# Kernel optimization log

Hardware: AMD Instinct MI355X
Metric: run time of the kernel (lower is better)

## Reference

```python
import jax, jax.numpy as jnp
from jax import lax
import numpy as np

ROUTINGS = 3
NUM_CAPSULE = 8
NUM_ATOMS = 32

def _squash(x):
    # squash(x) = x/||x|| * ||x||^2/(1+||x||^2), norm over last axis
    norm = jnp.linalg.norm(x, axis=-1, keepdims=True)
    norm_sq = norm * norm
    return x / norm * (norm_sq / (1.0 + norm_sq))

def setup_inputs() -> dict:
    key = jax.random.key(0)
    k1, k2, k3 = jax.random.split(key, 3)
    input_tensor = jax.random.normal(k1, (2, 24, 24, 24, 8, 32), dtype=jnp.float32)
    # he_normal-ish scale for conv kernel [k,k,k,in_atoms, C*A]
    fan_in = 3 * 3 * 3 * 32
    W = jax.random.normal(k2, (3, 3, 3, 32, NUM_CAPSULE * NUM_ATOMS), dtype=jnp.float32) * np.sqrt(2.0 / fan_in).astype(np.float32)
    b = jnp.full((1, 1, 1, NUM_CAPSULE, NUM_ATOMS), 0.1, dtype=jnp.float32)
    return {"input_tensor": input_tensor, "W": W, "b": b}

def reference(input_tensor, W, b):
    B, H, Wd, T, IC, IA = input_tensor.shape
    C, A = NUM_CAPSULE, NUM_ATOMS
    # fold input capsule dim into batch: [IC, B, H, W, T, IA] -> [IC*B, H, W, T, IA]
    x = jnp.transpose(input_tensor, (4, 0, 1, 2, 3, 5)).reshape(IC * B, H, Wd, T, IA)
    conv = lax.conv_general_dilated(
        x, W, window_strides=(1, 1, 1), padding='SAME',
        dimension_numbers=('NDHWC', 'DHWIO', 'NDHWC'))  # [IC*B, H, W, T, C*A]
    # reshape exactly as the TF layer does (leading dims relabelled [B, IC])
    votes = conv.reshape(B, IC, H, Wd, T, C, A)
    biases = jnp.broadcast_to(b, (H, Wd, T, C, A))
    logits = jnp.zeros((B, IC, H, Wd, T, C), dtype=votes.dtype)
    activation = None
    for i in range(ROUTINGS):
        route = jax.nn.softmax(logits, axis=-1)                     # [B,IC,H,W,T,C]
        # sum over input capsules of route-weighted votes, plus bias
        preactivate = jnp.sum(route[..., None] * votes, axis=1) + biases  # [B,H,W,T,C,A]
        activation = _squash(preactivate)
        if i < ROUTINGS - 1:
            # agreement update (last-iteration update never affects output)
            distances = jnp.sum(votes * activation[:, None], axis=-1)  # [B,IC,H,W,T,C]
            logits = logits + distances
    return activation
```

## Files before the change

kernel.cpp:

```cpp
#include <hip/hip_runtime.h>
#include <math.h>


#define SPT 13824

typedef __attribute__((ext_vector_type(8))) _Float16 half8;
typedef __attribute__((ext_vector_type(4))) float f32x4;

__device__ __forceinline__ float redhalf(float v) {
  v += __shfl_xor(v, 16);
  v += __shfl_xor(v, 8);
  v += __shfl_xor(v, 4);
  v += __shfl_xor(v, 2);
  v += __shfl_xor(v, 1);
  return v;
}

__global__ void prep_W(const float* __restrict__ W, _Float16* __restrict__ Wh) {
  const int tap = blockIdx.x;
  #pragma unroll
  for (int rep = 0; rep < 4; ++rep) {
    const int idx = rep * 256 + threadIdx.x;
    const int cb = idx >> 6;
    const int kg = (idx >> 4) & 3;
    const int nr = idx & 15;
    const int n  = cb * 16 + nr;
    half8 o;
    #pragma unroll
    for (int j = 0; j < 8; ++j)
      o[j] = (_Float16)W[(tap * 32 + kg * 8 + j) * 256 + n];
    *(half8*)(Wh + tap * 8192 + idx * 8) = o;
  }
}

__global__ __launch_bounds__(256, 4)
void caps_conv(const float* __restrict__ xg, const _Float16* __restrict__ Wh,
               _Float16* __restrict__ vws) {
  __shared__ __align__(16) unsigned char lds[34560];

  const int t    = threadIdx.x;
  const int lane = t & 63;
  const int w    = t >> 6;
  const int wg   = (blockIdx.x & 7) * 432 + (blockIdx.x >> 3);
  const int rbase = wg * 8;
  const int b2   = rbase / SPT;
  const int posb = rbase % SPT;
  const int z  = posb / 576;
  const int y  = (posb % 576) / 24;
  const int x0 = posb % 24;

  const bool stager = t < 240;
  const int sdy  = t / 80;
  const int srem = t % 80;
  const int sxs  = srem >> 3;
  const int sic  = srem & 7;
  const int sn   = b2 * 8 + sic;
  const int sbin = sn & 1;
  const int sicin = sn >> 1;
  const int syy  = y + sdy - 1;
  const int sxx  = x0 + sxs - 1;
  const int sR   = (sdy * 10 + sxs) * 8 + sic;
  const bool syx_ok = (unsigned)syy < 24u && (unsigned)sxx < 24u;
  const float* sbase = xg + (((sbin * 24) * 24 + (syx_ok ? syy : 0)) * 24 + (syx_ok ? sxx : 0)) * 256 + sicin * 32;

  const int lm = lane & 15;
  int abase[4];
  #pragma unroll
  for (int mi = 0; mi < 4; ++mi)
    abase[mi] = ((mi * 2 + (lm >> 3)) * 8 + (lane & 7)) * 72 + (lane >> 4) * 16;

  const _Float16* bbase = Wh + w * 2048 + lane * 8;

  f32x4 acc[4][4];
  #pragma unroll
  for (int mi = 0; mi < 4; ++mi)
    #pragma unroll
    for (int ni = 0; ni < 4; ++ni) acc[mi][ni] = (f32x4){0.f, 0.f, 0.f, 0.f};

  {
    const int zz = z - 1;
    const bool val = (unsigned)zz < 24u && syx_ok;
    const float* src = sbase + (zz >= 0 ? zz : 0) * 24 * 24 * 256;
    half8 h[4];
    #pragma unroll
    for (int j = 0; j < 4; ++j) {
      float4 qa = val ? *(const float4*)(src + j * 8)     : (float4){0,0,0,0};
      float4 qb = val ? *(const float4*)(src + j * 8 + 4) : (float4){0,0,0,0};
      half8 hh;
      hh[0]=(_Float16)qa.x; hh[1]=(_Float16)qa.y; hh[2]=(_Float16)qa.z; hh[3]=(_Float16)qa.w;
      hh[4]=(_Float16)qb.x; hh[5]=(_Float16)qb.y; hh[6]=(_Float16)qb.z; hh[7]=(_Float16)qb.w;
      h[j] = hh;
    }
    if (stager) {
      unsigned char* dst = lds + sR * 72;
      #pragma unroll
      for (int j = 0; j < 4; ++j) *(half8*)(dst + j * 16) = h[j];
    }
  }
  __syncthreads();

  #pragma unroll 1
  for (int dz = 0; dz < 3; ++dz) {
    half8 h[4];
    const bool have = dz < 2;
    {
      const int zz = z + dz;
      const bool val = have && (unsigned)zz < 24u && syx_ok;
      const float* src = sbase + zz * 24 * 24 * 256;
      #pragma unroll
      for (int j = 0; j < 4; ++j) {
        float4 qa = val ? *(const float4*)(src + j * 8)     : (float4){0,0,0,0};
        float4 qb = val ? *(const float4*)(src + j * 8 + 4) : (float4){0,0,0,0};
        half8 hh;
        hh[0]=(_Float16)qa.x; hh[1]=(_Float16)qa.y; hh[2]=(_Float16)qa.z; hh[3]=(_Float16)qa.w;
        hh[4]=(_Float16)qb.x; hh[5]=(_Float16)qb.y; hh[6]=(_Float16)qb.z; hh[7]=(_Float16)qb.w;
        h[j] = hh;
      }
    }

    const unsigned char* sb = lds + (dz & 1) * 17280;
    #pragma unroll 1
    for (int dy = 0; dy < 3; ++dy) {
      const _Float16* bt = bbase + (dz * 9 + dy * 3) * 8192;
      half8 bA0, bA1, bA2, bA3, bB0, bB1, bB2, bB3;
      bA0 = *(const half8*)(bt + 0 * 512);
      bA1 = *(const half8*)(bt + 1 * 512);
      bA2 = *(const half8*)(bt + 2 * 512);
      bA3 = *(const half8*)(bt + 3 * 512);

      bB0 = *(const half8*)(bt + 8192 + 0 * 512);
      bB1 = *(const half8*)(bt + 8192 + 1 * 512);
      bB2 = *(const half8*)(bt + 8192 + 2 * 512);
      bB3 = *(const half8*)(bt + 8192 + 3 * 512);
      {
        const int imm = dy * 5760;
        half8 af[4];
        #pragma unroll
        for (int mi = 0; mi < 4; ++mi) af[mi] = *(const half8*)(sb + abase[mi] + imm);
        #pragma unroll
        for (int mi = 0; mi < 4; ++mi) {
          acc[mi][0] = __builtin_amdgcn_mfma_f32_16x16x32_f16(af[mi], bA0, acc[mi][0], 0, 0, 0);
          acc[mi][1] = __builtin_amdgcn_mfma_f32_16x16x32_f16(af[mi], bA1, acc[mi][1], 0, 0, 0);
          acc[mi][2] = __builtin_amdgcn_mfma_f32_16x16x32_f16(af[mi], bA2, acc[mi][2], 0, 0, 0);
          acc[mi][3] = __builtin_amdgcn_mfma_f32_16x16x32_f16(af[mi], bA3, acc[mi][3], 0, 0, 0);
        }
      }
      bA0 = *(const half8*)(bt + 16384 + 0 * 512);
      bA1 = *(const half8*)(bt + 16384 + 1 * 512);
      bA2 = *(const half8*)(bt + 16384 + 2 * 512);
      bA3 = *(const half8*)(bt + 16384 + 3 * 512);
      {
        const int imm = dy * 5760 + 576;
        half8 af[4];
        #pragma unroll
        for (int mi = 0; mi < 4; ++mi) af[mi] = *(const half8*)(sb + abase[mi] + imm);
        #pragma unroll
        for (int mi = 0; mi < 4; ++mi) {
          acc[mi][0] = __builtin_amdgcn_mfma_f32_16x16x32_f16(af[mi], bB0, acc[mi][0], 0, 0, 0);
          acc[mi][1] = __builtin_amdgcn_mfma_f32_16x16x32_f16(af[mi], bB1, acc[mi][1], 0, 0, 0);
          acc[mi][2] = __builtin_amdgcn_mfma_f32_16x16x32_f16(af[mi], bB2, acc[mi][2], 0, 0, 0);
          acc[mi][3] = __builtin_amdgcn_mfma_f32_16x16x32_f16(af[mi], bB3, acc[mi][3], 0, 0, 0);
        }
      }
      {
        const int imm = dy * 5760 + 1152;
        half8 af[4];
        #pragma unroll
        for (int mi = 0; mi < 4; ++mi) af[mi] = *(const half8*)(sb + abase[mi] + imm);
        #pragma unroll
        for (int mi = 0; mi < 4; ++mi) {
          acc[mi][0] = __builtin_amdgcn_mfma_f32_16x16x32_f16(af[mi], bA0, acc[mi][0], 0, 0, 0);
          acc[mi][1] = __builtin_amdgcn_mfma_f32_16x16x32_f16(af[mi], bA1, acc[mi][1], 0, 0, 0);
          acc[mi][2] = __builtin_amdgcn_mfma_f32_16x16x32_f16(af[mi], bA2, acc[mi][2], 0, 0, 0);
          acc[mi][3] = __builtin_amdgcn_mfma_f32_16x16x32_f16(af[mi], bA3, acc[mi][3], 0, 0, 0);
        }
      }
    }

    if (have && stager) {
      unsigned char* dst = lds + ((dz + 1) & 1) * 17280 + sR * 72;
      #pragma unroll
      for (int j = 0; j < 4; ++j) *(half8*)(dst + j * 16) = h[j];
    }
    __syncthreads();
  }

  _Float16* vb = vws + (size_t)wg * 64 * 256;
  const int rowb = (lane >> 4) * 4;
  const int colb = w * 64 + (lane & 15);
  #pragma unroll
  for (int mi = 0; mi < 4; ++mi)
    #pragma unroll
    for (int ni = 0; ni < 4; ++ni)
      #pragma unroll
      for (int j = 0; j < 4; ++j)
        vb[(size_t)(mi * 16 + rowb + j) * 256 + colb + ni * 16] = (_Float16)acc[mi][ni][j];
}

__global__
void caps_route(const _Float16* __restrict__ vws, const float* __restrict__ bg,
                float* __restrict__ outg) {
  __shared__ float smL[4 * 128];

  const int t    = threadIdx.x;
  const int lane = t & 63;
  const int w    = t >> 6;
  const int grow = blockIdx.x * 4 + w;

  const int ch = lane >> 5;
  const int al = lane & 31;
  float* smLw = smL + w * 128;

  float bia[4];
  #pragma unroll
  for (int q = 0; q < 4; ++q) bia[q] = bg[(2 * q + ch) * 32 + al];

  const _Float16* vp = vws + (size_t)grow * 8 * 256;
  float v[8][4];
  #pragma unroll
  for (int ic = 0; ic < 8; ++ic)
    #pragma unroll
    for (int q = 0; q < 4; ++q)
      v[ic][q] = (float)vp[ic * 256 + (2 * q + ch) * 32 + al];

  #pragma unroll 1
  for (int it = 0; it < 3; ++it) {
    const float* Lrd = smLw + ((it + 1) & 1) * 64;
    float pre[4];
    #pragma unroll
    for (int q = 0; q < 4; ++q) pre[q] = bia[q];
    if (it == 0) {
      #pragma unroll
      for (int ic = 0; ic < 8; ++ic)
        #pragma unroll
        for (int q = 0; q < 4; ++q)
          pre[q] = fmaf(0.125f, v[ic][q], pre[q]);
    } else {
      #pragma unroll
      for (int ic = 0; ic < 8; ++ic) {
        const float4 La = *(const float4*)(Lrd + ic * 8);
        const float4 Lb = *(const float4*)(Lrd + ic * 8 + 4);
        const float Lv[8] = {La.x, La.y, La.z, La.w, Lb.x, Lb.y, Lb.z, Lb.w};
        float mx = Lv[0];
        #pragma unroll
        for (int cc = 1; cc < 8; ++cc) mx = fmaxf(mx, Lv[cc]);
        float e[8];
        float s = 0.f;
        #pragma unroll
        for (int cc = 0; cc < 8; ++cc) { e[cc] = __expf(Lv[cc] - mx); s += e[cc]; }
        const float inv = 1.0f / s;
        #pragma unroll
        for (int q = 0; q < 4; ++q)
          pre[q] = fmaf(e[2 * q + ch] * inv, v[ic][q], pre[q]);
      }
    }

    float act[4];
    #pragma unroll
    for (int q = 0; q < 4; ++q) {
      float ns = redhalf(pre[q] * pre[q]);
      act[q] = pre[q] * (sqrtf(ns) / (1.0f + ns));
    }

    if (it == 2) {
      #pragma unroll
      for (int q = 0; q < 4; ++q)
        outg[(size_t)grow * 256 + (2 * q + ch) * 32 + al] = act[q];
    } else {
      float* Lwr = smLw + (it & 1) * 64;
      #pragma unroll
      for (int ic = 0; ic < 8; ++ic)
        #pragma unroll
        for (int q = 0; q < 4; ++q) {
          float dd = redhalf(v[ic][q] * act[q]);
          if (al == 0) {
            const int cc = 2 * q + ch;
            Lwr[ic * 8 + cc] = (it == 0) ? dd : Lrd[ic * 8 + cc] + dd;
          }
        }
      __syncthreads();
    }
  }
}

__global__ __launch_bounds__(256, 4)
void caps_mfma7(const float* __restrict__ xg, const _Float16* __restrict__ Wh,
                const float* __restrict__ bg, float* __restrict__ outg) {
  __shared__ __align__(16) unsigned char lds[35840];
  float* smV = (float*)lds;

  const int t    = threadIdx.x;
  const int lane = t & 63;
  const int w    = t >> 6;
  const int wg   = (blockIdx.x & 7) * 432 + (blockIdx.x >> 3);
  const int rbase = wg * 8;
  const int b2   = rbase / SPT;
  const int posb = rbase % SPT;
  const int z  = posb / 576;
  const int y  = (posb % 576) / 24;
  const int x0 = posb % 24;

  const bool stager = t < 240;
  const int sdy  = t / 80;
  const int srem = t % 80;
  const int sxs  = srem >> 3;
  const int sic  = srem & 7;
  const int sn   = b2 * 8 + sic;
  const int sbin = sn & 1;
  const int sicin = sn >> 1;
  const int syy  = y + sdy - 1;
  const int sxx  = x0 + sxs - 1;
  const int sR   = (sdy * 10 + sxs) * 8 + sic;
  const bool syx_ok = (unsigned)syy < 24u && (unsigned)sxx < 24u;
  const float* sbase = xg + (((sbin * 24) * 24 + (syx_ok ? syy : 0)) * 24 + (syx_ok ? sxx : 0)) * 256 + sicin * 32;

  const int lm = lane & 15;
  int abase[4];
  #pragma unroll
  for (int mi = 0; mi < 4; ++mi)
    abase[mi] = ((mi * 2 + (lm >> 3)) * 8 + (lane & 7)) * 72 + (lane >> 4) * 16;

  const _Float16* bbase = Wh + w * 2048 + lane * 8;

  f32x4 acc[4][4];
  #pragma unroll
  for (int mi = 0; mi < 4; ++mi)
    #pragma unroll
    for (int ni = 0; ni < 4; ++ni) acc[mi][ni] = (f32x4){0.f, 0.f, 0.f, 0.f};

  {
    const int zz = z - 1;
    const bool val = (unsigned)zz < 24u && syx_ok;
    const float* src = sbase + (zz >= 0 ? zz : 0) * 24 * 24 * 256;
    half8 h[4];
    #pragma unroll
    for (int j = 0; j < 4; ++j) {
      float4 qa = val ? *(const float4*)(src + j * 8)     : (float4){0,0,0,0};
      float4 qb = val ? *(const float4*)(src + j * 8 + 4) : (float4){0,0,0,0};
      half8 hh;
      hh[0]=(_Float16)qa.x; hh[1]=(_Float16)qa.y; hh[2]=(_Float16)qa.z; hh[3]=(_Float16)qa.w;
      hh[4]=(_Float16)qb.x; hh[5]=(_Float16)qb.y; hh[6]=(_Float16)qb.z; hh[7]=(_Float16)qb.w;
      h[j] = hh;
    }
    if (stager) {
      unsigned char* dst = lds + sR * 72;
      #pragma unroll
      for (int j = 0; j < 4; ++j) *(half8*)(dst + j * 16) = h[j];
    }
  }
  __syncthreads();

  #pragma unroll 1
  for (int dz = 0; dz < 3; ++dz) {
    half8 h[4];
    const bool have = dz < 2;
    {
      const int zz = z + dz;
      const bool val = have && (unsigned)zz < 24u && syx_ok;
      const float* src = sbase + zz * 24 * 24 * 256;
      #pragma unroll
      for (int j = 0; j < 4; ++j) {
        float4 qa = val ? *(const float4*)(src + j * 8)     : (float4){0,0,0,0};
        float4 qb = val ? *(const float4*)(src + j * 8 + 4) : (float4){0,0,0,0};
        half8 hh;
        hh[0]=(_Float16)qa.x; hh[1]=(_Float16)qa.y; hh[2]=(_Float16)qa.z; hh[3]=(_Float16)qa.w;
        hh[4]=(_Float16)qb.x; hh[5]=(_Float16)qb.y; hh[6]=(_Float16)qb.z; hh[7]=(_Float16)qb.w;
        h[j] = hh;
      }
    }

    const unsigned char* sb = lds + (dz & 1) * 17280;
    #pragma unroll 1
    for (int dy = 0; dy < 3; ++dy) {
      const _Float16* bt = bbase + (dz * 9 + dy * 3) * 8192;
      half8 bA0, bA1, bA2, bA3, bB0, bB1, bB2, bB3;
      bA0 = *(const half8*)(bt + 0 * 512);
      bA1 = *(const half8*)(bt + 1 * 512);
      bA2 = *(const half8*)(bt + 2 * 512);
      bA3 = *(const half8*)(bt + 3 * 512);

      bB0 = *(const half8*)(bt + 8192 + 0 * 512);
      bB1 = *(const half8*)(bt + 8192 + 1 * 512);
      bB2 = *(const half8*)(bt + 8192 + 2 * 512);
      bB3 = *(const half8*)(bt + 8192 + 3 * 512);
      {
        const int imm = dy * 5760;
        half8 af[4];
        #pragma unroll
        for (int mi = 0; mi < 4; ++mi) af[mi] = *(const half8*)(sb + abase[mi] + imm);
        #pragma unroll
        for (int mi = 0; mi < 4; ++mi) {
          acc[mi][0] = __builtin_amdgcn_mfma_f32_16x16x32_f16(af[mi], bA0, acc[mi][0], 0, 0, 0);
          acc[mi][1] = __builtin_amdgcn_mfma_f32_16x16x32_f16(af[mi], bA1, acc[mi][1], 0, 0, 0);
          acc[mi][2] = __builtin_amdgcn_mfma_f32_16x16x32_f16(af[mi], bA2, acc[mi][2], 0, 0, 0);
          acc[mi][3] = __builtin_amdgcn_mfma_f32_16x16x32_f16(af[mi], bA3, acc[mi][3], 0, 0, 0);
        }
      }
      bA0 = *(const half8*)(bt + 16384 + 0 * 512);
      bA1 = *(const half8*)(bt + 16384 + 1 * 512);
      bA2 = *(const half8*)(bt + 16384 + 2 * 512);
      bA3 = *(const half8*)(bt + 16384 + 3 * 512);
      {
        const int imm = dy * 5760 + 576;
        half8 af[4];
        #pragma unroll
        for (int mi = 0; mi < 4; ++mi) af[mi] = *(const half8*)(sb + abase[mi] + imm);
        #pragma unroll
        for (int mi = 0; mi < 4; ++mi) {
          acc[mi][0] = __builtin_amdgcn_mfma_f32_16x16x32_f16(af[mi], bB0, acc[mi][0], 0, 0, 0);
          acc[mi][1] = __builtin_amdgcn_mfma_f32_16x16x32_f16(af[mi], bB1, acc[mi][1], 0, 0, 0);
          acc[mi][2] = __builtin_amdgcn_mfma_f32_16x16x32_f16(af[mi], bB2, acc[mi][2], 0, 0, 0);
          acc[mi][3] = __builtin_amdgcn_mfma_f32_16x16x32_f16(af[mi], bB3, acc[mi][3], 0, 0, 0);
        }
      }
      {
        const int imm = dy * 5760 + 1152;
        half8 af[4];
        #pragma unroll
        for (int mi = 0; mi < 4; ++mi) af[mi] = *(const half8*)(sb + abase[mi] + imm);
        #pragma unroll
        for (int mi = 0; mi < 4; ++mi) {
          acc[mi][0] = __builtin_amdgcn_mfma_f32_16x16x32_f16(af[mi], bA0, acc[mi][0], 0, 0, 0);
          acc[mi][1] = __builtin_amdgcn_mfma_f32_16x16x32_f16(af[mi], bA1, acc[mi][1], 0, 0, 0);
          acc[mi][2] = __builtin_amdgcn_mfma_f32_16x16x32_f16(af[mi], bA2, acc[mi][2], 0, 0, 0);
          acc[mi][3] = __builtin_amdgcn_mfma_f32_16x16x32_f16(af[mi], bA3, acc[mi][3], 0, 0, 0);
        }
      }
    }

    if (have && stager) {
      unsigned char* dst = lds + ((dz + 1) & 1) * 17280 + sR * 72;
      #pragma unroll
      for (int j = 0; j < 4; ++j) *(half8*)(dst + j * 16) = h[j];
    }
    __syncthreads();
  }

  const int ch = lane >> 5;
  const int al = lane & 31;
  float* smLw = (float*)(lds + 33792) + w * 128;

  float bia[4];
  #pragma unroll
  for (int q = 0; q < 4; ++q) bia[q] = bg[(2 * q + ch) * 32 + al];

  #pragma unroll 1
  for (int pass = 0; pass < 2; ++pass) {
    #pragma unroll
    for (int mh = 0; mh < 2; ++mh) {
      const int mi = pass * 2 + mh;
      #pragma unroll
      for (int ni = 0; ni < 4; ++ni) {
        #pragma unroll
        for (int j = 0; j < 4; ++j) {
          const int rl  = mh * 16 + (lane >> 4) * 4 + j;
          const int col = w * 64 + ni * 16 + (lane & 15);
          smV[rl * 264 + col] = acc[mi][ni][j];
        }
      }
    }
    __syncthreads();

    float v[8][4];
    #pragma unroll
    for (int ic = 0; ic < 8; ++ic)
      #pragma unroll
      for (int q = 0; q < 4; ++q)
        v[ic][q] = smV[(w * 8 + ic) * 264 + (2 * q + ch) * 32 + al];

    #pragma unroll 1
    for (int it = 0; it < 3; ++it) {
      const float* Lrd = smLw + ((it + 1) & 1) * 64;
      float pre[4];
      #pragma unroll
      for (int q = 0; q < 4; ++q) pre[q] = bia[q];
      if (it == 0) {
        #pragma unroll
        for (int ic = 0; ic < 8; ++ic)
          #pragma unroll
          for (int q = 0; q < 4; ++q)
            pre[q] = fmaf(0.125f, v[ic][q], pre[q]);
      } else {
        #pragma unroll
        for (int ic = 0; ic < 8; ++ic) {
          const float4 La = *(const float4*)(Lrd + ic * 8);
          const float4 Lb = *(const float4*)(Lrd + ic * 8 + 4);
          const float Lv[8] = {La.x, La.y, La.z, La.w, Lb.x, Lb.y, Lb.z, Lb.w};
          float mx = Lv[0];
          #pragma unroll
          for (int cc = 1; cc < 8; ++cc) mx = fmaxf(mx, Lv[cc]);
          float e[8];
          float s = 0.f;
          #pragma unroll
          for (int cc = 0; cc < 8; ++cc) { e[cc] = __expf(Lv[cc] - mx); s += e[cc]; }
          const float inv = 1.0f / s;
          #pragma unroll
          for (int q = 0; q < 4; ++q)
            pre[q] = fmaf(e[2 * q + ch] * inv, v[ic][q], pre[q]);
        }
      }

      float act[4];
      #pragma unroll
      for (int q = 0; q < 4; ++q) {
        float ns = redhalf(pre[q] * pre[q]);
        act[q] = pre[q] * (sqrtf(ns) / (1.0f + ns));
      }

      if (it == 2) {
        const int pl = pass * 4 + w;
        #pragma unroll
        for (int q = 0; q < 4; ++q)
          outg[(rbase + pl) * 256 + (2 * q + ch) * 32 + al] = act[q];
      } else {
        float* Lwr = smLw + (it & 1) * 64;
        #pragma unroll
        for (int ic = 0; ic < 8; ++ic)
          #pragma unroll
          for (int q = 0; q < 4; ++q) {
            float dd = redhalf(v[ic][q] * act[q]);
            if (al == 0) {
              const int cc = 2 * q + ch;
              Lwr[ic * 8 + cc] = (it == 0) ? dd : Lrd[ic * 8 + cc] + dd;
            }
          }
        __syncthreads();
      }
    }
  }
}

__global__ __launch_bounds__(256, 3)
void caps_fused(const float* __restrict__ xg, const float* __restrict__ Wg,
                const float* __restrict__ bg, float* __restrict__ outg) {
  __shared__ __align__(16) float sm[10432];
  float* smA = sm;
  float* smB = sm + 2176;
  float* smV = sm;
  float* smL = sm + 10368;

  const int t    = threadIdx.x;
  const int blk  = blockIdx.x;
  const int rbase = blk * 8;
  const int b2   = rbase / SPT;
  const int posb = rbase % SPT;
  const int z  = posb / 576;
  const int y  = (posb % 576) / 24;
  const int x0 = posb % 24;

  const int pix_t = t >> 4;
  const int oc_t  = t & 15;
  const int am    = t >> 2;
  const int acin  = (t & 3) * 8;
  const int a_pl  = am >> 3;
  const int a_n   = b2 * 8 + (am & 7);
  const int a_bin = a_n & 1;
  const int a_icin = a_n >> 1;

  float acc[4][16];
  #pragma unroll
  for (int i = 0; i < 4; ++i)
    #pragma unroll
    for (int j = 0; j < 16; ++j) acc[i][j] = 0.f;

  #pragma unroll 1
  for (int tap = 0; tap < 27; ++tap) {
    const int dz = tap / 9, dy = (tap % 9) / 3, dx = tap % 3;
    const int zz = z + dz - 1;
    const int yy = y + dy - 1;
    const int xx = x0 + a_pl + dx - 1;

    float4 va = {0.f, 0.f, 0.f, 0.f}, vb = {0.f, 0.f, 0.f, 0.f};
    if ((unsigned)zz < 24u && (unsigned)yy < 24u && (unsigned)xx < 24u) {
      const float* src = xg + ((((a_bin * 24 + zz) * 24 + yy) * 24 + xx) * 8 + a_icin) * 32 + acin;
      va = *(const float4*)src;
      vb = *(const float4*)(src + 4);
    }
    float4 wv[8];
    const float* wsrc = Wg + tap * 8192 + t * 4;
    #pragma unroll
    for (int k = 0; k < 8; ++k) wv[k] = *(const float4*)(wsrc + k * 1024);

    __syncthreads();
    smA[(acin + 0) * 68 + am] = va.x;
    smA[(acin + 1) * 68 + am] = va.y;
    smA[(acin + 2) * 68 + am] = va.z;
    smA[(acin + 3) * 68 + am] = va.w;
    smA[(acin + 4) * 68 + am] = vb.x;
    smA[(acin + 5) * 68 + am] = vb.y;
    smA[(acin + 6) * 68 + am] = vb.z;
    smA[(acin + 7) * 68 + am] = vb.w;
    #pragma unroll
    for (int k = 0; k < 8; ++k) *(float4*)&smB[k * 1024 + t * 4] = wv[k];
    __syncthreads();

    #pragma unroll 8
    for (int cin = 0; cin < 32; ++cin) {
      const float4 a4  = *(const float4*)&smA[cin * 68 + pix_t * 4];
      const float4 b0  = *(const float4*)&smB[cin * 256 + oc_t * 4];
      const float4 b1  = *(const float4*)&smB[cin * 256 + oc_t * 4 + 64];
      const float4 b2v = *(const float4*)&smB[cin * 256 + oc_t * 4 + 128];
      const float4 b3v = *(const float4*)&smB[cin * 256 + oc_t * 4 + 192];
      const float ar[4] = {a4.x, a4.y, a4.z, a4.w};
      #pragma unroll
      for (int i = 0; i < 4; ++i) {
        acc[i][0]  = fmaf(ar[i], b0.x,  acc[i][0]);
        acc[i][1]  = fmaf(ar[i], b0.y,  acc[i][1]);
        acc[i][2]  = fmaf(ar[i], b0.z,  acc[i][2]);
        acc[i][3]  = fmaf(ar[i], b0.w,  acc[i][3]);
        acc[i][4]  = fmaf(ar[i], b1.x,  acc[i][4]);
        acc[i][5]  = fmaf(ar[i], b1.y,  acc[i][5]);
        acc[i][6]  = fmaf(ar[i], b1.z,  acc[i][6]);
        acc[i][7]  = fmaf(ar[i], b1.w,  acc[i][7]);
        acc[i][8]  = fmaf(ar[i], b2v.x, acc[i][8]);
        acc[i][9]  = fmaf(ar[i], b2v.y, acc[i][9]);
        acc[i][10] = fmaf(ar[i], b2v.z, acc[i][10]);
        acc[i][11] = fmaf(ar[i], b2v.w, acc[i][11]);
        acc[i][12] = fmaf(ar[i], b3v.x, acc[i][12]);
        acc[i][13] = fmaf(ar[i], b3v.y, acc[i][13]);
        acc[i][14] = fmaf(ar[i], b3v.z, acc[i][14]);
        acc[i][15] = fmaf(ar[i], b3v.w, acc[i][15]);
      }
    }
  }
  __syncthreads();

  const int c = t >> 5;
  const int a = t & 31;
  const float bia = bg[t];

  #pragma unroll 1
  for (int pass = 0; pass < 2; ++pass) {
    if ((pix_t >> 3) == pass) {
      const int rl = (pix_t & 7) * 4;
      #pragma unroll
      for (int i = 0; i < 4; ++i) {
        #pragma unroll
        for (int jj = 0; jj < 4; ++jj) {
          float4 v4 = {acc[i][jj * 4 + 0], acc[i][jj * 4 + 1],
                       acc[i][jj * 4 + 2], acc[i][jj * 4 + 3]};
          *(float4*)&smV[(rl + i) * 256 + oc_t * 4 + jj * 64] = v4;
        }
      }
    }
    __syncthreads();

    #pragma unroll 1
    for (int pp = 0; pp < 4; ++pp) {
      const int pl = pass * 4 + pp;
      float v[8];
      #pragma unroll
      for (int ic = 0; ic < 8; ++ic) v[ic] = smV[(pp * 8 + ic) * 256 + t];

      float route[8];
      #pragma unroll 1
      for (int it = 0; it < 3; ++it) {
        if (it == 0) {
          #pragma unroll
          for (int ic = 0; ic < 8; ++ic) route[ic] = 0.125f;
        } else {
          #pragma unroll
          for (int ic = 0; ic < 8; ++ic) {
            float mx = -3.4e38f;
            #pragma unroll
            for (int cc = 0; cc < 8; ++cc) mx = fmaxf(mx, smL[ic * 8 + cc]);
            float s = 0.f;
            #pragma unroll
            for (int cc = 0; cc < 8; ++cc) s += __expf(smL[ic * 8 + cc] - mx);
            route[ic] = __expf(smL[ic * 8 + c] - mx) / s;
          }
        }
        float pre = bia;
        #pragma unroll
        for (int ic = 0; ic < 8; ++ic) pre = fmaf(route[ic], v[ic], pre);

        float ns = redhalf(pre * pre);
        const float nrm = sqrtf(ns);
        const float act = pre * (nrm / (1.0f + ns));

        if (it == 2) {
          outg[(rbase + pl) * 256 + t] = act;
        } else {
          float d[8];
          #pragma unroll
          for (int ic = 0; ic < 8; ++ic) d[ic] = redhalf(v[ic] * act);
          __syncthreads();
          if (a == 0) {
            #pragma unroll
            for (int ic = 0; ic < 8; ++ic)
              smL[ic * 8 + c] = (it == 0) ? d[ic] : smL[ic * 8 + c] + d[ic];
          }
          __syncthreads();
        }
      }
    }
    __syncthreads();
  }
}

extern "C" void kernel_launch(void* const* d_in, const int* in_sizes, int n_in,
                              void* d_out, int out_size, void* d_ws, size_t ws_size,
                              hipStream_t stream) {
  const float* x = (const float*)d_in[0];
  const float* W = (const float*)d_in[1];
  const float* b = (const float*)d_in[2];
  float* out = (float*)d_out;
  (void)in_sizes; (void)n_in; (void)out_size;

  const size_t need_wh    = 27u * 8192u * sizeof(_Float16);
  const size_t need_split = need_wh + (size_t)27648 * 2048 * sizeof(_Float16);

  if (ws_size >= need_split) {
    _Float16* Wh  = (_Float16*)d_ws;
    _Float16* vws = (_Float16*)((unsigned char*)d_ws + need_wh);
    prep_W<<<dim3(27), dim3(256), 0, stream>>>(W, Wh);
    caps_conv<<<dim3(3456), dim3(256), 0, stream>>>(x, Wh, vws);
    caps_route<<<dim3(6912), dim3(256), 0, stream>>>(vws, b, out);
  } else if (ws_size >= need_wh) {
    _Float16* Wh = (_Float16*)d_ws;
    prep_W<<<dim3(27), dim3(256), 0, stream>>>(W, Wh);
    caps_mfma7<<<dim3(3456), dim3(256), 0, stream>>>(x, Wh, b, out);
  } else {
    caps_fused<<<dim3(3456), dim3(256), 0, stream>>>(x, W, b, out);
  }
}
```

Before: 337.6 us.

## Split conv output channels across two blocks and single-buffer LDS

The conv kernel now splits the 256 output channels into two halves handled by separate workgroups, doubling the grid and halving the per-wave accumulator and B-fragment registers. The LDS tile is single-buffered with an extra barrier before and after each refill, which halves shared memory per block, and launch bounds are raised to allow 5 blocks per CU. The aim is higher occupancy and more parallelism. The cost is that each input tile is staged and converted twice, and the load/compute overlap from double buffering is lost.

```diff
diff --git a/kernel.cpp b/kernel.cpp
--- a/kernel.cpp
+++ b/kernel.cpp
@@ -33,15 +33,17 @@
   }
 }
 
-__global__ __launch_bounds__(256, 4)
-void caps_conv(const float* __restrict__ xg, const _Float16* __restrict__ Wh,
-               _Float16* __restrict__ vws) {
-  __shared__ __align__(16) unsigned char lds[34560];
+__global__ __launch_bounds__(256, 5)
+void caps_conv2(const float* __restrict__ xg, const _Float16* __restrict__ Wh,
+                _Float16* __restrict__ vws) {
+  __shared__ __align__(16) unsigned char lds[17280];
 
   const int t    = threadIdx.x;
   const int lane = t & 63;
   const int w    = t >> 6;
-  const int wg   = (blockIdx.x & 7) * 432 + (blockIdx.x >> 3);
+  const int bid  = (blockIdx.x & 7) * 864 + (blockIdx.x >> 3);
+  const int wg   = bid >> 1;
+  const int nh   = bid & 1;
   const int rbase = wg * 8;
   const int b2   = rbase / SPT;
   const int posb = rbase % SPT;
@@ -69,13 +71,13 @@
   for (int mi = 0; mi < 4; ++mi)
     abase[mi] = ((mi * 2 + (lm >> 3)) * 8 + (lane & 7)) * 72 + (lane >> 4) * 16;
 
-  const _Float16* bbase = Wh + w * 2048 + lane * 8;
-
-  f32x4 acc[4][4];
+  const _Float16* bbase = Wh + (nh * 8 + w * 2) * 512 + lane * 8;
+
+  f32x4 acc[4][2];
   #pragma unroll
   for (int mi = 0; mi < 4; ++mi)
     #pragma unroll
-    for (int ni = 0; ni < 4; ++ni) acc[mi][ni] = (f32x4){0.f, 0.f, 0.f, 0.f};
+    for (int ni = 0; ni < 2; ++ni) acc[mi][ni] = (f32x4){0.f, 0.f, 0.f, 0.f};
 
   {
     const int zz = z - 1;
@@ -118,20 +120,16 @@
       }
     }
 
-    const unsigned char* sb = lds + (dz & 1) * 17280;
+    const unsigned char* sb = lds;
     #pragma unroll 1
     for (int dy = 0; dy < 3; ++dy) {
       const _Float16* bt = bbase + (dz * 9 + dy * 3) * 8192;
-      half8 bA0, bA1, bA2, bA3, bB0, bB1, bB2, bB3;
-      bA0 = *(const half8*)(bt + 0 * 512);
-      bA1 = *(const half8*)(bt + 1 * 512);
-      bA2 = *(const half8*)(bt + 2 * 512);
-      bA3 = *(const half8*)(bt + 3 * 512);
-
-      bB0 = *(const half8*)(bt + 8192 + 0 * 512);
-      bB1 = *(const half8*)(bt + 8192 + 1 * 512);
-      bB2 = *(const half8*)(bt + 8192 + 2 * 512);
-      bB3 = *(const half8*)(bt + 8192 + 3 * 512);
+      half8 bP0, bP1, bQ0, bQ1;
+      bP0 = *(const half8*)(bt + 0 * 512);
+      bP1 = *(const half8*)(bt + 1 * 512);
+
+      bQ0 = *(const half8*)(bt + 8192 + 0 * 512);
+      bQ1 = *(const half8*)(bt + 8192 + 1 * 512);
       {
         const int imm = dy * 5760;
         half8 af[4];
@@ -139,16 +137,12 @@
         for (int mi = 0; mi < 4; ++mi) af[mi] = *(const half8*)(sb + abase[mi] + imm);
         #pragma unroll
         for (int mi = 0; mi < 4; ++mi) {
-          acc[mi][0] = __builtin_amdgcn_mfma_f32_16x16x32_f16(af[mi], bA0, acc[mi][0], 0, 0, 0);
-          acc[mi][1] = __builtin_amdgcn_mfma_f32_16x16x32_f16(af[mi], bA1, acc[mi][1], 0, 0, 0);
-          acc[mi][2] = __builtin_amdgcn_mfma_f32_16x16x32_f16(af[mi], bA2, acc[mi][2], 0, 0, 0);
-          acc[mi][3] = __builtin_amdgcn_mfma_f32_16x16x32_f16(af[mi], bA3, acc[mi][3], 0, 0, 0);
-        }
-      }
-      bA0 = *(const half8*)(bt + 16384 + 0 * 512);
-      bA1 = *(const half8*)(bt + 16384 + 1 * 512);
-      bA2 = *(const half8*)(bt + 16384 + 2 * 512);
-      bA3 = *(const half8*)(bt + 16384 + 3 * 512);
+          acc[mi][0] = __builtin_amdgcn_mfma_f32_16x16x32_f16(af[mi], bP0, acc[mi][0], 0, 0, 0);
+          acc[mi][1] = __builtin_amdgcn_mfma_f32_16x16x32_f16(af[mi], bP1, acc[mi][1], 0, 0, 0);
+        }
+      }
+      bP0 = *(const half8*)(bt + 16384 + 0 * 512);
+      bP1 = *(const half8*)(bt + 16384 + 1 * 512);
       {
         const int imm = dy * 5760 + 576;
         half8 af[4];
@@ -156,10 +150,8 @@
         for (int mi = 0; mi < 4; ++mi) af[mi] = *(const half8*)(sb + abase[mi] + imm);
         #pragma unroll
         for (int mi = 0; mi < 4; ++mi) {
-          acc[mi][0] = __builtin_amdgcn_mfma_f32_16x16x32_f16(af[mi], bB0, acc[mi][0], 0, 0, 0);
-          acc[mi][1] = __builtin_amdgcn_mfma_f32_16x16x32_f16(af[mi], bB1, acc[mi][1], 0, 0, 0);
-          acc[mi][2] = __builtin_amdgcn_mfma_f32_16x16x32_f16(af[mi], bB2, acc[mi][2], 0, 0, 0);
-          acc[mi][3] = __builtin_amdgcn_mfma_f32_16x16x32_f16(af[mi], bB3, acc[mi][3], 0, 0, 0);
+          acc[mi][0] = __builtin_amdgcn_mfma_f32_16x16x32_f16(af[mi], bQ0, acc[mi][0], 0, 0, 0);
+          acc[mi][1] = __builtin_amdgcn_mfma_f32_16x16x32_f16(af[mi], bQ1, acc[mi][1], 0, 0, 0);
         }
       }
       {
@@ -169,29 +161,30 @@
         for (int mi = 0; mi < 4; ++mi) af[mi] = *(const half8*)(sb + abase[mi] + imm);
         #pragma unroll
         for (int mi = 0; mi < 4; ++mi) {
-          acc[mi][0] = __builtin_amdgcn_mfma_f32_16x16x32_f16(af[mi], bA0, acc[mi][0], 0, 0, 0);
-          acc[mi][1] = __builtin_amdgcn_mfma_f32_16x16x32_f16(af[mi], bA1, acc[mi][1], 0, 0, 0);
-          acc[mi][2] = __builtin_amdgcn_mfma_f32_16x16x32_f16(af[mi], bA2, acc[mi][2], 0, 0, 0);
-          acc[mi][3] = __builtin_amdgcn_mfma_f32_16x16x32_f16(af[mi], bA3, acc[mi][3], 0, 0, 0);
-        }
-      }
-    }
-
-    if (have && stager) {
-      unsigned char* dst = lds + ((dz + 1) & 1) * 17280 + sR * 72;
-      #pragma unroll
-      for (int j = 0; j < 4; ++j) *(half8*)(dst + j * 16) = h[j];
-    }
+          acc[mi][0] = __builtin_amdgcn_mfma_f32_16x16x32_f16(af[mi], bP0, acc[mi][0], 0, 0, 0);
+          acc[mi][1] = __builtin_amdgcn_mfma_f32_16x16x32_f16(af[mi], bP1, acc[mi][1], 0, 0, 0);
+        }
+      }
+    }
+
     __syncthreads();
+    if (have) {
+      if (stager) {
+        unsigned char* dst = lds + sR * 72;
+        #pragma unroll
+        for (int j = 0; j < 4; ++j) *(half8*)(dst + j * 16) = h[j];
+      }
+      __syncthreads();
+    }
   }
 
   _Float16* vb = vws + (size_t)wg * 64 * 256;
   const int rowb = (lane >> 4) * 4;
-  const int colb = w * 64 + (lane & 15);
+  const int colb = nh * 128 + w * 32 + (lane & 15);
   #pragma unroll
   for (int mi = 0; mi < 4; ++mi)
     #pragma unroll
-    for (int ni = 0; ni < 4; ++ni)
+    for (int ni = 0; ni < 2; ++ni)
       #pragma unroll
       for (int j = 0; j < 4; ++j)
         vb[(size_t)(mi * 16 + rowb + j) * 256 + colb + ni * 16] = (_Float16)acc[mi][ni][j];
@@ -714,7 +707,7 @@
     _Float16* Wh  = (_Float16*)d_ws;
     _Float16* vws = (_Float16*)((unsigned char*)d_ws + need_wh);
     prep_W<<<dim3(27), dim3(256), 0, stream>>>(W, Wh);
-    caps_conv<<<dim3(3456), dim3(256), 0, stream>>>(x, Wh, vws);
+    caps_conv2<<<dim3(6912), dim3(256), 0, stream>>>(x, Wh, vws);
     caps_route<<<dim3(6912), dim3(256), 0, stream>>>(vws, b, out);
   } else if (ws_size >= need_wh) {
     _Float16* Wh = (_Float16*)d_ws;
```

New measurement: 458.4 us. +35.8%, slower.
